# Kernel tuning notes

Measured on AMD Instinct MI355X. Metric: run time of the kernel, lower is better.

## Reference

```python
import jax, jax.numpy as jnp
import numpy as np
import math

B, T, D = 48, 4096, 256
K_TIMES = 1
# replicate torch module's stage/block computation (static Python math)
_ns = (int(math.log(T)) + 1) * K_TIMES          # 9
BLOCK = int(T / _ns)                             # 455
if T % _ns != 0:
    N_STAGES = int(T / BLOCK) + 1                # 10
    PAD = N_STAGES * BLOCK - T                   # 454
else:
    N_STAGES, PAD = _ns, 0


def setup_inputs() -> dict:
    key = jax.random.key(0)
    k1, k2 = jax.random.split(key)
    x = jax.random.normal(k1, (B, T, D), dtype=jnp.float32)
    # fusion linear: in=2D, out=D (torch Linear weight [out,in])
    W_fuse = jax.random.normal(k2, (D, 2 * D), dtype=jnp.float32) * (1.0 / np.sqrt(2 * D))
    b_fuse = jnp.zeros((D,), dtype=jnp.float32)
    return {"x": x, "W_fuse": W_fuse, "b_fuse": b_fuse}


def _attention(q, k, v):
    # q: [..., Lq, D], k/v: [..., Lk, D]
    scores = jnp.matmul(q, jnp.swapaxes(k, -2, -1)) / jnp.sqrt(jnp.asarray(q.shape[-1], q.dtype))
    p = jax.nn.softmax(scores, axis=-1)
    return jnp.matmul(p, v)


def reference(x, W_fuse, b_fuse):
    xp = jnp.pad(x, ((0, 0), (0, PAD), (0, 0)))                      # [B, N_STAGES*BLOCK, D]
    chunked = xp.reshape(B * N_STAGES, BLOCK, D)                      # [B*S, BLOCK, D]
    q = jnp.max(chunked, axis=1).reshape(B, N_STAGES, D)              # block summaries [B, S, D]
    q_block = _attention(q, q, q)                                     # [B, S, D]
    q_step = _attention(q_block.reshape(B * N_STAGES, 1, D), chunked, chunked)
    q_step = q_step.reshape(B, N_STAGES, D)                           # [B, S, D]
    fused = jnp.concatenate([q_block, q_step], axis=-1)               # [B, S, 2D]
    return jnp.einsum('bsf,df->bsd', fused, W_fuse) + b_fuse
```

## Files before the change

### kernel.cpp

```cpp
#include <hip/hip_runtime.h>
#include <math.h>

#define NB 48
#define NT 4096
#define ND 256
#define NS 10
#define BLK 455
#define NP 4
#define RPP 114

__global__ __launch_bounds__(256) void kmaxp(const float* __restrict__ x,
                                             float* __restrict__ qpart) {
    const int bsp = blockIdx.x;
    const int p  = bsp & 3;
    const int bs = bsp >> 2;
    const int b = bs / NS, s = bs % NS;
    const int start = p * RPP;
    const int len   = min(BLK - start, RPP);
    const int nrows = min(BLK, NT - s * BLK);
    const int nreal = max(0, min(nrows - start, len));
    const int npad  = len - nreal;
    const int g = threadIdx.x & 63;
    const int w = threadIdx.x >> 6;
    const long base = ((long)b * NT + (long)s * BLK + start) * ND;

    float4 m = (npad > 0) ? make_float4(0.f, 0.f, 0.f, 0.f)
                          : make_float4(-INFINITY, -INFINITY, -INFINITY, -INFINITY);
    for (int r = w; r < nreal; r += 4) {
        const float4 v = *reinterpret_cast<const float4*>(x + base + (long)r * ND + g * 4);
        m.x = fmaxf(m.x, v.x); m.y = fmaxf(m.y, v.y);
        m.z = fmaxf(m.z, v.z); m.w = fmaxf(m.w, v.w);
    }

    __shared__ float4 red[4][64];
    red[w][g] = m;
    __syncthreads();
    if (w == 0) {
        float4 a = red[0][g];
        #pragma unroll
        for (int k = 1; k < 4; ++k) {
            const float4 o = red[k][g];
            a.x = fmaxf(a.x, o.x); a.y = fmaxf(a.y, o.y);
            a.z = fmaxf(a.z, o.z); a.w = fmaxf(a.w, o.w);
        }
        *reinterpret_cast<float4*>(qpart + (long)bsp * ND + g * 4) = a;
    }
}

__global__ __launch_bounds__(256) void kqblock(const float* __restrict__ qpart,
                                               float* __restrict__ qb) {
    const int b = blockIdx.x;
    const int tid = threadIdx.x;
    __shared__ float sq[NS][ND];
    __shared__ float sp[NS][NS];

    for (int i = tid; i < NS * ND; i += 256) {
        const int st = i / ND, d = i % ND;
        const long base = ((long)(b * NS + st) * NP) * ND + d;
        float v = qpart[base];
        #pragma unroll
        for (int p = 1; p < NP; ++p) v = fmaxf(v, qpart[base + (long)p * ND]);
        sq[st][d] = v;
    }
    __syncthreads();

    if (tid < NS * NS) {
        const int i = tid / NS, j = tid % NS;
        float acc = 0.f;
        for (int d = 0; d < ND; ++d) acc += sq[i][d] * sq[j][d];
        sp[i][j] = acc * 0.0625f;
    }
    __syncthreads();

    if (tid < NS) {
        float m = -INFINITY;
        for (int j = 0; j < NS; ++j) m = fmaxf(m, sp[tid][j]);
        float sum = 0.f;
        for (int j = 0; j < NS; ++j) { const float e = expf(sp[tid][j] - m); sp[tid][j] = e; sum += e; }
        const float inv = 1.f / sum;
        for (int j = 0; j < NS; ++j) sp[tid][j] *= inv;
    }
    __syncthreads();

    for (int i = 0; i < NS; ++i) {
        float acc = 0.f;
        #pragma unroll
        for (int j = 0; j < NS; ++j) acc += sp[i][j] * sq[j][tid];
        qb[((long)b * NS + i) * ND + tid] = acc;
    }
}

__global__ __launch_bounds__(256) void kstepp(const float* __restrict__ x,
                                              const float* __restrict__ qb,
                                              float* __restrict__ mpart,
                                              float* __restrict__ lpart,
                                              float* __restrict__ accpart) {
    const int bsp = blockIdx.x;
    const int p  = bsp & 3;
    const int bs = bsp >> 2;
    const int b = bs / NS, s = bs % NS;
    const int start = p * RPP;
    const int len   = min(BLK - start, RPP);
    const int nrows = min(BLK, NT - s * BLK);
    const int nreal = max(0, min(nrows - start, len));
    const int npad  = len - nreal;
    const int lane = threadIdx.x & 63;
    const int w    = threadIdx.x >> 6;
    const long base = ((long)b * NT + (long)s * BLK + start) * ND;

    const float4 qb4 = *reinterpret_cast<const float4*>(qb + (long)bs * ND + lane * 4);

    float m = -INFINITY, l = 0.f;
    float4 acc = make_float4(0.f, 0.f, 0.f, 0.f);

    for (int r = w; r < nreal; r += 4) {
        const float4 v = *reinterpret_cast<const float4*>(x + base + (long)r * ND + lane * 4);
        float sc = v.x * qb4.x + v.y * qb4.y + v.z * qb4.z + v.w * qb4.w;
        #pragma unroll
        for (int o = 32; o; o >>= 1) sc += __shfl_xor(sc, o);
        sc *= 0.0625f;
        if (sc > m) {
            const float g = expf(m - sc);
            l *= g; acc.x *= g; acc.y *= g; acc.z *= g; acc.w *= g;
            m = sc;
        }
        const float e = expf(sc - m);
        l += e;
        acc.x += e * v.x; acc.y += e * v.y;
        acc.z += e * v.z; acc.w += e * v.w;
    }

    __shared__ float  sm[4], sl[4];
    __shared__ float4 sacc[4][64];
    if (lane == 0) { sm[w] = m; sl[w] = l; }
    sacc[w][lane] = acc;
    __syncthreads();

    if (w == 0) {
        float mp = (npad > 0) ? 0.f : -INFINITY;
        #pragma unroll
        for (int k = 0; k < 4; ++k) mp = fmaxf(mp, sm[k]);
        float lf = (float)npad * expf(-mp);
        float4 af = make_float4(0.f, 0.f, 0.f, 0.f);
        #pragma unroll
        for (int k = 0; k < 4; ++k) {
            const float g = expf(sm[k] - mp);
            lf += sl[k] * g;
            const float4 o = sacc[k][lane];
            af.x += o.x * g; af.y += o.y * g;
            af.z += o.z * g; af.w += o.w * g;
        }
        if (lane == 0) { mpart[bsp] = mp; lpart[bsp] = lf; }
        *reinterpret_cast<float4*>(accpart + (long)bsp * ND + lane * 4) = af;
    }
}

__global__ __launch_bounds__(256) void kfinal(const float* __restrict__ qb,
                                              const float* __restrict__ mpart,
                                              const float* __restrict__ lpart,
                                              const float* __restrict__ accpart,
                                              const float* __restrict__ Wf,
                                              const float* __restrict__ bf,
                                              float* __restrict__ out) {
    const int bs = blockIdx.x;
    const int d = threadIdx.x;

    const float m0 = mpart[bs * NP + 0], m1 = mpart[bs * NP + 1];
    const float m2 = mpart[bs * NP + 2], m3 = mpart[bs * NP + 3];
    const float mm = fmaxf(fmaxf(m0, m1), fmaxf(m2, m3));
    const float s0 = expf(m0 - mm), s1 = expf(m1 - mm);
    const float s2 = expf(m2 - mm), s3 = expf(m3 - mm);
    const float l = lpart[bs * NP + 0] * s0 + lpart[bs * NP + 1] * s1
                  + lpart[bs * NP + 2] * s2 + lpart[bs * NP + 3] * s3;
    const float a = accpart[((long)bs * NP + 0) * ND + d] * s0
                  + accpart[((long)bs * NP + 1) * ND + d] * s1
                  + accpart[((long)bs * NP + 2) * ND + d] * s2
                  + accpart[((long)bs * NP + 3) * ND + d] * s3;
    const float qs = a / l;

    __shared__ float f[2 * ND];
    f[d]      = qb[(long)bs * ND + d];
    f[ND + d] = qs;
    __syncthreads();

    const float* wr = Wf + (long)d * 2 * ND;
    float acc = bf[d];
    for (int k = 0; k < 2 * ND; k += 4) {
        const float4 w4 = *reinterpret_cast<const float4*>(wr + k);
        acc += f[k] * w4.x + f[k + 1] * w4.y + f[k + 2] * w4.z + f[k + 3] * w4.w;
    }
    out[(long)bs * ND + d] = acc;
}

extern "C" void kernel_launch(void* const* d_in, const int* in_sizes, int n_in,
                              void* d_out, int out_size, void* d_ws, size_t ws_size,
                              hipStream_t stream) {
    const float* x  = (const float*)d_in[0];
    const float* Wf = (const float*)d_in[1];
    const float* bf = (const float*)d_in[2];
    float* out = (float*)d_out;

    float* qpart   = (float*)d_ws;
    float* accpart = qpart + NB * NS * NP * ND;
    float* qb      = accpart + NB * NS * NP * ND;
    float* mpart   = qb + NB * NS * ND;
    float* lpart   = mpart + NB * NS * NP;

    kmaxp  <<<NB * NS * NP, 256, 0, stream>>>(x, qpart);
    kqblock<<<NB,           256, 0, stream>>>(qpart, qb);
    kstepp <<<NB * NS * NP, 256, 0, stream>>>(x, qb, mpart, lpart, accpart);
    kfinal <<<NB * NS,      256, 0, stream>>>(qb, mpart, lpart, accpart, Wf, bf, out);
}
```

Before: 350.6 us.

## Batch four rows per iteration in step attention and reuse weights across eight rows

The online-softmax loop in kstepp now loads four rows per warp per iteration and interleaves their shuffle reductions, which raises memory-level parallelism and shortens the serial shuffle chain. The final linear kernel processes eight (b,s) rows per block, so each weight row is loaded once and reused across eight outputs instead of being reread per row. A guard is added so that partitions with no real rows merge safely. The trade-off is fewer blocks in the final kernel (60) and more registers in kstepp.

```diff
diff --git a/kernel.cpp b/kernel.cpp
--- a/kernel.cpp
+++ b/kernel.cpp
@@ -8,6 +8,7 @@
 #define BLK 455
 #define NP 4
 #define RPP 114
+#define RPB 8
 
 __global__ __launch_bounds__(256) void kmaxp(const float* __restrict__ x,
                                              float* __restrict__ qpart) {
@@ -113,21 +114,49 @@
     float m = -INFINITY, l = 0.f;
     float4 acc = make_float4(0.f, 0.f, 0.f, 0.f);
 
-    for (int r = w; r < nreal; r += 4) {
-        const float4 v = *reinterpret_cast<const float4*>(x + base + (long)r * ND + lane * 4);
-        float sc = v.x * qb4.x + v.y * qb4.y + v.z * qb4.z + v.w * qb4.w;
-        #pragma unroll
-        for (int o = 32; o; o >>= 1) sc += __shfl_xor(sc, o);
-        sc *= 0.0625f;
-        if (sc > m) {
-            const float g = expf(m - sc);
-            l *= g; acc.x *= g; acc.y *= g; acc.z *= g; acc.w *= g;
-            m = sc;
-        }
-        const float e = expf(sc - m);
-        l += e;
-        acc.x += e * v.x; acc.y += e * v.y;
-        acc.z += e * v.z; acc.w += e * v.w;
+    if (nreal > 0) {
+        for (int k = 0; k < (RPP + 15) / 16; ++k) {
+            const int r0 = k * 16 + w * 4;
+            if (r0 >= nreal && k > 0) break;
+            float4 v0, v1, v2, v3;
+            float p0, p1, p2, p3;
+            const int c0 = min(r0 + 0, nreal - 1);
+            const int c1 = min(r0 + 1, nreal - 1);
+            const int c2 = min(r0 + 2, nreal - 1);
+            const int c3 = min(r0 + 3, nreal - 1);
+            v0 = *reinterpret_cast<const float4*>(x + base + (long)c0 * ND + lane * 4);
+            v1 = *reinterpret_cast<const float4*>(x + base + (long)c1 * ND + lane * 4);
+            v2 = *reinterpret_cast<const float4*>(x + base + (long)c2 * ND + lane * 4);
+            v3 = *reinterpret_cast<const float4*>(x + base + (long)c3 * ND + lane * 4);
+            p0 = v0.x * qb4.x + v0.y * qb4.y + v0.z * qb4.z + v0.w * qb4.w;
+            p1 = v1.x * qb4.x + v1.y * qb4.y + v1.z * qb4.z + v1.w * qb4.w;
+            p2 = v2.x * qb4.x + v2.y * qb4.y + v2.z * qb4.z + v2.w * qb4.w;
+            p3 = v3.x * qb4.x + v3.y * qb4.y + v3.z * qb4.z + v3.w * qb4.w;
+            #pragma unroll
+            for (int o = 32; o; o >>= 1) {
+                p0 += __shfl_xor(p0, o);
+                p1 += __shfl_xor(p1, o);
+                p2 += __shfl_xor(p2, o);
+                p3 += __shfl_xor(p3, o);
+            }
+            const float scs[4] = { p0 * 0.0625f, p1 * 0.0625f, p2 * 0.0625f, p3 * 0.0625f };
+            const float4 vs[4] = { v0, v1, v2, v3 };
+            #pragma unroll
+            for (int j = 0; j < 4; ++j) {
+                if (r0 + j < nreal) {
+                    const float sc = scs[j];
+                    if (sc > m) {
+                        const float g = expf(m - sc);
+                        l *= g; acc.x *= g; acc.y *= g; acc.z *= g; acc.w *= g;
+                        m = sc;
+                    }
+                    const float e = expf(sc - m);
+                    l += e;
+                    acc.x += e * vs[j].x; acc.y += e * vs[j].y;
+                    acc.z += e * vs[j].z; acc.w += e * vs[j].w;
+                }
+            }
+        }
     }
 
     __shared__ float  sm[4], sl[4];
@@ -144,7 +173,7 @@
         float4 af = make_float4(0.f, 0.f, 0.f, 0.f);
         #pragma unroll
         for (int k = 0; k < 4; ++k) {
-            const float g = expf(sm[k] - mp);
+            const float g = (sm[k] == -INFINITY) ? 0.f : expf(sm[k] - mp);
             lf += sl[k] * g;
             const float4 o = sacc[k][lane];
             af.x += o.x * g; af.y += o.y * g;
@@ -155,41 +184,53 @@
     }
 }
 
-__global__ __launch_bounds__(256) void kfinal(const float* __restrict__ qb,
-                                              const float* __restrict__ mpart,
-                                              const float* __restrict__ lpart,
-                                              const float* __restrict__ accpart,
-                                              const float* __restrict__ Wf,
-                                              const float* __restrict__ bf,
-                                              float* __restrict__ out) {
-    const int bs = blockIdx.x;
+__global__ __launch_bounds__(256) void kfinal8(const float* __restrict__ qb,
+                                               const float* __restrict__ mpart,
+                                               const float* __restrict__ lpart,
+                                               const float* __restrict__ accpart,
+                                               const float* __restrict__ Wf,
+                                               const float* __restrict__ bf,
+                                               float* __restrict__ out) {
+    const int blk = blockIdx.x;
     const int d = threadIdx.x;
-
-    const float m0 = mpart[bs * NP + 0], m1 = mpart[bs * NP + 1];
-    const float m2 = mpart[bs * NP + 2], m3 = mpart[bs * NP + 3];
-    const float mm = fmaxf(fmaxf(m0, m1), fmaxf(m2, m3));
-    const float s0 = expf(m0 - mm), s1 = expf(m1 - mm);
-    const float s2 = expf(m2 - mm), s3 = expf(m3 - mm);
-    const float l = lpart[bs * NP + 0] * s0 + lpart[bs * NP + 1] * s1
-                  + lpart[bs * NP + 2] * s2 + lpart[bs * NP + 3] * s3;
-    const float a = accpart[((long)bs * NP + 0) * ND + d] * s0
-                  + accpart[((long)bs * NP + 1) * ND + d] * s1
-                  + accpart[((long)bs * NP + 2) * ND + d] * s2
-                  + accpart[((long)bs * NP + 3) * ND + d] * s3;
-    const float qs = a / l;
-
-    __shared__ float f[2 * ND];
-    f[d]      = qb[(long)bs * ND + d];
-    f[ND + d] = qs;
-    __syncthreads();
+    __shared__ float f[RPB][2 * ND];
+
+    #pragma unroll
+    for (int j = 0; j < RPB; ++j) {
+        const int bs = blk * RPB + j;
+        const float m0 = mpart[bs * NP + 0], m1 = mpart[bs * NP + 1];
+        const float m2 = mpart[bs * NP + 2], m3 = mpart[bs * NP + 3];
+        const float mm = fmaxf(fmaxf(m0, m1), fmaxf(m2, m3));
+        const float s0 = expf(m0 - mm), s1 = expf(m1 - mm);
+        const float s2 = expf(m2 - mm), s3 = expf(m3 - mm);
+        const float l = lpart[bs * NP + 0] * s0 + lpart[bs * NP + 1] * s1
+                      + lpart[bs * NP + 2] * s2 + lpart[bs * NP + 3] * s3;
+        const float a = accpart[((long)bs * NP + 0) * ND + d] * s0
+                      + accpart[((long)bs * NP + 1) * ND + d] * s1
+                      + accpart[((long)bs * NP + 2) * ND + d] * s2
+                      + accpart[((long)bs * NP + 3) * ND + d] * s3;
+        f[j][d]      = qb[(long)bs * ND + d];
+        f[j][ND + d] = a / l;
+    }
+    __syncthreads();
+
+    float acc[RPB];
+    const float bias = bf[d];
+    #pragma unroll
+    for (int j = 0; j < RPB; ++j) acc[j] = bias;
 
     const float* wr = Wf + (long)d * 2 * ND;
-    float acc = bf[d];
     for (int k = 0; k < 2 * ND; k += 4) {
         const float4 w4 = *reinterpret_cast<const float4*>(wr + k);
-        acc += f[k] * w4.x + f[k + 1] * w4.y + f[k + 2] * w4.z + f[k + 3] * w4.w;
-    }
-    out[(long)bs * ND + d] = acc;
+        #pragma unroll
+        for (int j = 0; j < RPB; ++j) {
+            const float4 fj = *reinterpret_cast<const float4*>(&f[j][k]);
+            acc[j] += fj.x * w4.x + fj.y * w4.y + fj.z * w4.z + fj.w * w4.w;
+        }
+    }
+    #pragma unroll
+    for (int j = 0; j < RPB; ++j)
+        out[(long)(blk * RPB + j) * ND + d] = acc[j];
 }
 
 extern "C" void kernel_launch(void* const* d_in, const int* in_sizes, int n_in,
@@ -209,5 +250,5 @@
     kmaxp  <<<NB * NS * NP, 256, 0, stream>>>(x, qpart);
     kqblock<<<NB,           256, 0, stream>>>(qpart, qb);
     kstepp <<<NB * NS * NP, 256, 0, stream>>>(x, qb, mpart, lpart, accpart);
-    kfinal <<<NB * NS,      256, 0, stream>>>(qb, mpart, lpart, accpart, Wf, bf, out);
-}
+    kfinal8<<<NB * NS / RPB, 256, 0, stream>>>(qb, mpart, lpart, accpart, Wf, bf, out);
+}
```

Result: no change. 351.4 us (+0.2%).
